# Optimization experiments

Measured on AMD Instinct MI355X. Metric: run time of the kernel, lower is better.

Reference implementation:

```python
import jax, jax.numpy as jnp
import numpy as np

BETA = 0.9
THRESHOLD = 0.9
SIM_TIME = 100

@jax.custom_vjp
def spike(u):
    # snntorch ATan surrogate spike: forward heaviside, backward 1/(1+(pi*u)^2) (alpha=2)
    return (u > 0).astype(u.dtype)

def _spike_fwd(u):
    return (u > 0).astype(u.dtype), u

def _spike_bwd(u, g):
    return (g / (1.0 + (jnp.pi * u) ** 2),)

spike.defvjp(_spike_fwd, _spike_bwd)

def setup_inputs() -> dict:
    key = jax.random.key(0)
    k1, k2, k3 = jax.random.split(key, 3)
    B, D, H = 2048, 1024, 256
    x = jax.random.normal(k1, (B, D), dtype=jnp.float32)
    enc_w = jax.random.normal(k2, (D, H), dtype=jnp.float32) * 0.1
    dec_w = jax.random.normal(k3, (H, D), dtype=jnp.float32) * 0.1
    return {"x": x, "enc_w": enc_w, "dec_w": dec_w}

def _snn_forward(x, enc_w, dec_w):
    B = x.shape[0]
    D, H = enc_w.shape
    dt = x.dtype
    # input current is constant across timesteps (x fixed); hoist the matmul
    in_cur = x @ enc_w  # [B, H]

    def step(carry, _):
        # NOTE: original repo swaps snntorch's (spk, mem) return, so the
        # carried "mem" state is actually the previous spike train, and the
        # membrane potential is what flows into the decoder matmul.
        s_e, s_d, _, _ = carry
        reset_e = jax.lax.stop_gradient((s_e > THRESHOLD).astype(dt))
        m_e = BETA * s_e + in_cur - reset_e * THRESHOLD          # [B, H]
        spk_e = spike(m_e - THRESHOLD)
        out_cur = m_e @ dec_w                                    # [B, D] (mem used as 'spikes')
        reset_d = jax.lax.stop_gradient((s_d > THRESHOLD).astype(dt))
        m_d = BETA * s_d + out_cur - reset_d * THRESHOLD         # [B, D]
        spk_d = spike(m_d - THRESHOLD)
        return (spk_e, spk_d, m_e, m_d), None

    init = (jnp.zeros((B, H), dt), jnp.zeros((B, D), dt),
            jnp.zeros((B, H), dt), jnp.zeros((B, D), dt))
    (s_e, s_d, m_e, m_d), _ = jax.lax.scan(step, init, None, length=SIM_TIME)
    # original returns (spikes_decoder, spikes_encoder) which hold the membranes
    return m_d, m_e

def reference(x, enc_w, dec_w):
    return _snn_forward(x, enc_w, dec_w)
```

## Files before the change

kernel.cpp:

```cpp
#include <hip/hip_runtime.h>


typedef __attribute__((ext_vector_type(8))) short bf16x8;
typedef __attribute__((ext_vector_type(4))) float f32x4;
typedef __attribute__((ext_vector_type(8))) unsigned short ushort8;

__device__ __forceinline__ unsigned short f2bf(float f) {
    unsigned u = __builtin_bit_cast(unsigned, f);
    unsigned r = u + 0x7FFFu + ((u >> 16) & 1u);
    return (unsigned short)(r >> 16);
}

__device__ __forceinline__ void gload_lds16(const void* src, void* dst) {
    __builtin_amdgcn_global_load_lds(
        (const __attribute__((address_space(1))) void*)src,
        (__attribute__((address_space(3))) void*)dst, 16, 0, 0);
}

template <int ROWS>
__device__ __forceinline__ void stage_tile(const unsigned short* __restrict__ g,
                                           int ld, unsigned short* lds, int t) {
    #pragma unroll
    for (int c = 0; c < ROWS / 32; ++c) {
        const int idx = c * 256 + t;
        const int row = idx >> 3;
        const int chunk = (idx & 7) ^ (row & 7);
        const unsigned short* src = g + (size_t)row * ld + chunk * 8;
        unsigned short* dst = lds + (size_t)(idx & ~63) * 8;
        gload_lds16(src, dst);
    }
}

__global__ __launch_bounds__(256) void gemm1_bk256(
    const unsigned short* __restrict__ A,
    const unsigned short* __restrict__ Bt,
    float* __restrict__ C,
    unsigned short* __restrict__ Cbf)
{
    constexpr int N = 256, K = 1024, BK = 256, NT = K / BK;
    __shared__ __align__(16) unsigned short As[2][32 * BK];
    __shared__ __align__(16) unsigned short Bs[2][32 * BK];

    const int t = threadIdx.x;
    const int lane = t & 63;
    const int l15 = lane & 15, l4 = lane >> 4;
    const int wid = t >> 6;
    const int wr = wid >> 1, wc = wid & 1;
    const int brow = blockIdx.y * 32, bcol = blockIdx.x * 32;

    const unsigned short* Ab = A + (size_t)brow * K;
    const unsigned short* Bb = Bt + (size_t)bcol * K;

    auto stage = [&](int kt, int buf) {
        #pragma unroll
        for (int c = 0; c < 4; ++c) {
            const int idx = c * 256 + t;
            const int row = idx >> 5;
            const int ch = (idx & 31) ^ (row & 31);
            gload_lds16(Ab + (size_t)row * K + kt * BK + ch * 8,
                        &As[buf][(idx & ~63) * 8]);
        }
        #pragma unroll
        for (int c = 0; c < 4; ++c) {
            const int idx = c * 256 + t;
            const int row = idx >> 5;
            const int ch = (idx & 31) ^ (row & 31);
            gload_lds16(Bb + (size_t)row * K + kt * BK + ch * 8,
                        &Bs[buf][(idx & ~63) * 8]);
        }
    };

    f32x4 acc = {0.f, 0.f, 0.f, 0.f};
    stage(0, 0);
    for (int kt = 0; kt < NT; ++kt) {
        __syncthreads();
        if (kt + 1 < NT) stage(kt + 1, (kt + 1) & 1);
        const unsigned short* Asb = As[kt & 1];
        const unsigned short* Bsb = Bs[kt & 1];
        const int ra = wr * 16 + l15;
        const int rb = wc * 16 + l15;
        #pragma unroll
        for (int s = 0; s < 8; ++s) {
            const int ca = (s * 4 + l4) ^ (ra & 31);
            const bf16x8 aF = *(const bf16x8*)&Asb[ra * BK + ca * 8];
            const int cb = (s * 4 + l4) ^ (rb & 31);
            const bf16x8 bF = *(const bf16x8*)&Bsb[rb * BK + cb * 8];
            acc = __builtin_amdgcn_mfma_f32_16x16x32_bf16(aF, bF, acc, 0, 0, 0);
        }
    }

    #pragma unroll
    for (int reg = 0; reg < 4; ++reg) {
        const int row = brow + wr * 16 + l4 * 4 + reg;
        const int col = bcol + wc * 16 + l15;
        const float v = acc[reg];
        C[(size_t)row * N + col] = v;
        Cbf[(size_t)row * N + col] = f2bf(v);
    }
}

__global__ __launch_bounds__(256) void gemm2_kres128(
    const unsigned short* __restrict__ A,
    const unsigned short* __restrict__ B,
    float* __restrict__ C)
{
    constexpr int K = 256, N = 1024;
    __shared__ __align__(16) unsigned short As[4][32 * 64];
    __shared__ __align__(16) unsigned short Bs[4][128 * 64];

    const int t = threadIdx.x;
    const int lane = t & 63;
    const int l15 = lane & 15, l4 = lane >> 4;
    const int wid = t >> 6;
    const int wr = wid >> 1, wc = wid & 1;
    const int brow = blockIdx.y * 32, bcol = blockIdx.x * 128;

    #pragma unroll
    for (int kt = 0; kt < 4; ++kt) {
        stage_tile<32>(A + (size_t)brow * K + kt * 64, K, As[kt], t);
        stage_tile<128>(B + (size_t)bcol * K + kt * 64, K, Bs[kt], t);
    }
    __syncthreads();

    f32x4 acc[4];
    #pragma unroll
    for (int j = 0; j < 4; ++j) acc[j] = {0.f, 0.f, 0.f, 0.f};

    #pragma unroll
    for (int kt = 0; kt < 4; ++kt)
        #pragma unroll
        for (int s = 0; s < 2; ++s) {
            const int ra = wr * 16 + l15;
            const int cha = (s * 4 + l4) ^ (ra & 7);
            const bf16x8 aF = *(const bf16x8*)&As[kt][ra * 64 + cha * 8];
            #pragma unroll
            for (int j = 0; j < 4; ++j) {
                const int rb = wc * 64 + j * 16 + l15;
                const int chb = (s * 4 + l4) ^ (rb & 7);
                const bf16x8 bF = *(const bf16x8*)&Bs[kt][rb * 64 + chb * 8];
                acc[j] = __builtin_amdgcn_mfma_f32_16x16x32_bf16(aF, bF, acc[j], 0, 0, 0);
            }
        }

    #pragma unroll
    for (int j = 0; j < 4; ++j)
        #pragma unroll
        for (int reg = 0; reg < 4; ++reg) {
            const int row = brow + wr * 16 + l4 * 4 + reg;
            const int col = bcol + wc * 64 + j * 16 + l15;
            C[(size_t)row * N + col] = acc[j][reg];
        }
}

__global__ __launch_bounds__(256) void prep(
    const float* __restrict__ x, const float* __restrict__ enc,
    const float* __restrict__ dec, unsigned short* __restrict__ x_bf,
    unsigned short* __restrict__ encT, unsigned short* __restrict__ decT)
{
    __shared__ unsigned short tile[32][33];
    const int bid = blockIdx.x;
    const int t = threadIdx.x;

    if (bid < 1024) {
        const int i = bid * 256 + t;
        float4 a = ((const float4*)x)[2 * i];
        float4 b = ((const float4*)x)[2 * i + 1];
        ushort8 v;
        v[0] = f2bf(a.x); v[1] = f2bf(a.y); v[2] = f2bf(a.z); v[3] = f2bf(a.w);
        v[4] = f2bf(b.x); v[5] = f2bf(b.y); v[6] = f2bf(b.z); v[7] = f2bf(b.w);
        ((ushort8*)x_bf)[i] = v;
        return;
    }
    const float* in; unsigned short* out; int R, C, bx, by;
    if (bid < 1280) {
        const int bb = bid - 1024;
        in = enc; out = encT; R = 1024; C = 256; bx = bb % 8; by = bb / 8;
    } else {
        const int bb = bid - 1280;
        in = dec; out = decT; R = 256; C = 1024; bx = bb % 32; by = bb / 32;
    }
    const int r0 = by * 32, c0 = bx * 32;
    const int tx = t % 32, ty = t / 32;
    #pragma unroll
    for (int k = 0; k < 4; ++k) {
        const int lr = ty + k * 8;
        tile[lr][tx] = f2bf(in[(size_t)(r0 + lr) * C + c0 + tx]);
    }
    __syncthreads();
    #pragma unroll
    for (int k = 0; k < 4; ++k) {
        const int lc = ty + k * 8;
        out[(size_t)(c0 + lc) * R + r0 + tx] = tile[tx][lc];
    }
}

#define BKF 32
#define PADF 4
template <int BM, int BN, int TM, int TN>
__global__ __launch_bounds__(256) void gemm_f32(
    const float* __restrict__ A, const float* __restrict__ B,
    float* __restrict__ C, int M, int N, int K)
{
    __shared__ float As[BKF][BM + PADF];
    __shared__ float Bs[BKF][BN + PADF];
    const int t = threadIdx.x;
    const int brow = blockIdx.y * BM, bcol = blockIdx.x * BN;
    constexpr int NTX = BN / TN;
    const int tx = t % NTX, ty = t / NTX;
    float acc[TM][TN];
    #pragma unroll
    for (int i = 0; i < TM; ++i)
        #pragma unroll
        for (int j = 0; j < TN; ++j) acc[i][j] = 0.f;
    for (int k0 = 0; k0 < K; k0 += BKF) {
        #pragma unroll
        for (int v = t; v < BM * BKF / 4; v += 256) {
            const int row = v / (BKF / 4), kv = v % (BKF / 4);
            const float4 val = *(const float4*)&A[(size_t)(brow + row) * K + k0 + kv * 4];
            As[kv * 4 + 0][row] = val.x; As[kv * 4 + 1][row] = val.y;
            As[kv * 4 + 2][row] = val.z; As[kv * 4 + 3][row] = val.w;
        }
        #pragma unroll
        for (int v = t; v < BKF * BN / 4; v += 256) {
            const int kk = v / (BN / 4), cv = v % (BN / 4);
            *(float4*)&Bs[kk][cv * 4] = *(const float4*)&B[(size_t)(k0 + kk) * N + bcol + cv * 4];
        }
        __syncthreads();
        #pragma unroll
        for (int k = 0; k < BKF; ++k) {
            float a[TM], b[TN];
            #pragma unroll
            for (int i = 0; i < TM; ++i) a[i] = As[k][ty * TM + i];
            #pragma unroll
            for (int j = 0; j < TN; ++j) b[j] = Bs[k][tx * TN + j];
            #pragma unroll
            for (int i = 0; i < TM; ++i)
                #pragma unroll
                for (int j = 0; j < TN; ++j) acc[i][j] = fmaf(a[i], b[j], acc[i][j]);
        }
        __syncthreads();
    }
    #pragma unroll
    for (int i = 0; i < TM; ++i)
        #pragma unroll
        for (int j = 0; j < TN; ++j)
            C[(size_t)(brow + ty * TM + i) * N + bcol + tx * TN + j] = acc[i][j];
}

extern "C" void kernel_launch(void* const* d_in, const int* in_sizes, int n_in,
                              void* d_out, int out_size, void* d_ws, size_t ws_size,
                              hipStream_t stream) {
    const float* x     = (const float*)d_in[0];
    const float* enc_w = (const float*)d_in[1];
    const float* dec_w = (const float*)d_in[2];

    const int B = 2048, D = 1024, H = 256;
    float* m_d = (float*)d_out;
    float* m_e = (float*)d_out + (size_t)B * D;

    const size_t need = (size_t)B * D * 2 + (size_t)D * H * 2 * 2 + (size_t)B * H * 2;
    if (ws_size >= need) {
        unsigned short* x_bf  = (unsigned short*)d_ws;
        unsigned short* encT  = x_bf + (size_t)B * D;
        unsigned short* decT  = encT + (size_t)H * D;
        unsigned short* me_bf = decT + (size_t)D * H;

        prep<<<dim3(1536), dim3(256), 0, stream>>>(x, enc_w, dec_w, x_bf, encT, decT);

        gemm1_bk256<<<dim3(H / 32, B / 32), dim3(256), 0, stream>>>(x_bf, encT, m_e, me_bf);
        gemm2_kres128<<<dim3(D / 128, B / 32), dim3(256), 0, stream>>>(me_bf, decT, m_d);
    } else {
        gemm_f32<64, 32, 4, 2><<<dim3(H / 32, B / 64), dim3(256), 0, stream>>>(x, enc_w, m_e, B, H, D);
        gemm_f32<64, 64, 4, 4><<<dim3(D / 64, B / 64), dim3(256), 0, stream>>>(m_e, dec_w, m_d, B, D, H);
    }
}
```

Measured before the change: 23.74 us.

## Fuse both GEMMs into a persistent kernel with per-strip dependency counters

The two GEMM launches become one 512-block kernel. Blocks take work tiles through atomic counters: first the encoder GEMM tiles, then the decoder GEMM tiles. Each decoder tile spins on a per-strip release/acquire counter until that strip's encoder output is complete, which lets the two stages overlap and removes a launch boundary. The cost is an extra memset launch, atomic traffic, a spin-wait dependency, and a larger 80KB static LDS allocation, which may reduce occupancy.

```diff
diff --git a/kernel.cpp b/kernel.cpp
--- a/kernel.cpp
+++ b/kernel.cpp
@@ -31,125 +31,152 @@
     }
 }
 
-__global__ __launch_bounds__(256) void gemm1_bk256(
-    const unsigned short* __restrict__ A,
-    const unsigned short* __restrict__ Bt,
-    float* __restrict__ C,
-    unsigned short* __restrict__ Cbf)
+__global__ __launch_bounds__(256) void fused12(
+    const unsigned short* __restrict__ x_bf,
+    const unsigned short* __restrict__ encT,
+    const unsigned short* __restrict__ decT,
+    float* __restrict__ m_e,
+    unsigned short* __restrict__ me_bf,
+    float* __restrict__ m_d,
+    unsigned int* __restrict__ ctr)
 {
-    constexpr int N = 256, K = 1024, BK = 256, NT = K / BK;
-    __shared__ __align__(16) unsigned short As[2][32 * BK];
-    __shared__ __align__(16) unsigned short Bs[2][32 * BK];
+    __shared__ __align__(16) unsigned char smem[81920];
+    volatile unsigned int* s_t = (volatile unsigned int*)smem;
 
     const int t = threadIdx.x;
     const int lane = t & 63;
     const int l15 = lane & 15, l4 = lane >> 4;
     const int wid = t >> 6;
     const int wr = wid >> 1, wc = wid & 1;
-    const int brow = blockIdx.y * 32, bcol = blockIdx.x * 32;
-
-    const unsigned short* Ab = A + (size_t)brow * K;
-    const unsigned short* Bb = Bt + (size_t)bcol * K;
-
-    auto stage = [&](int kt, int buf) {
-        #pragma unroll
-        for (int c = 0; c < 4; ++c) {
-            const int idx = c * 256 + t;
-            const int row = idx >> 5;
-            const int ch = (idx & 31) ^ (row & 31);
-            gload_lds16(Ab + (size_t)row * K + kt * BK + ch * 8,
-                        &As[buf][(idx & ~63) * 8]);
-        }
-        #pragma unroll
-        for (int c = 0; c < 4; ++c) {
-            const int idx = c * 256 + t;
-            const int row = idx >> 5;
-            const int ch = (idx & 31) ^ (row & 31);
-            gload_lds16(Bb + (size_t)row * K + kt * BK + ch * 8,
-                        &Bs[buf][(idx & ~63) * 8]);
-        }
-    };
-
-    f32x4 acc = {0.f, 0.f, 0.f, 0.f};
-    stage(0, 0);
-    for (int kt = 0; kt < NT; ++kt) {
-        __syncthreads();
-        if (kt + 1 < NT) stage(kt + 1, (kt + 1) & 1);
-        const unsigned short* Asb = As[kt & 1];
-        const unsigned short* Bsb = Bs[kt & 1];
-        const int ra = wr * 16 + l15;
-        const int rb = wc * 16 + l15;
-        #pragma unroll
-        for (int s = 0; s < 8; ++s) {
-            const int ca = (s * 4 + l4) ^ (ra & 31);
-            const bf16x8 aF = *(const bf16x8*)&Asb[ra * BK + ca * 8];
-            const int cb = (s * 4 + l4) ^ (rb & 31);
-            const bf16x8 bF = *(const bf16x8*)&Bsb[rb * BK + cb * 8];
-            acc = __builtin_amdgcn_mfma_f32_16x16x32_bf16(aF, bF, acc, 0, 0, 0);
-        }
-    }
-
-    #pragma unroll
-    for (int reg = 0; reg < 4; ++reg) {
-        const int row = brow + wr * 16 + l4 * 4 + reg;
-        const int col = bcol + wc * 16 + l15;
-        const float v = acc[reg];
-        C[(size_t)row * N + col] = v;
-        Cbf[(size_t)row * N + col] = f2bf(v);
-    }
-}
-
-__global__ __launch_bounds__(256) void gemm2_kres128(
-    const unsigned short* __restrict__ A,
-    const unsigned short* __restrict__ B,
-    float* __restrict__ C)
-{
-    constexpr int K = 256, N = 1024;
-    __shared__ __align__(16) unsigned short As[4][32 * 64];
-    __shared__ __align__(16) unsigned short Bs[4][128 * 64];
-
-    const int t = threadIdx.x;
-    const int lane = t & 63;
-    const int l15 = lane & 15, l4 = lane >> 4;
-    const int wid = t >> 6;
-    const int wr = wid >> 1, wc = wid & 1;
-    const int brow = blockIdx.y * 32, bcol = blockIdx.x * 128;
-
-    #pragma unroll
-    for (int kt = 0; kt < 4; ++kt) {
-        stage_tile<32>(A + (size_t)brow * K + kt * 64, K, As[kt], t);
-        stage_tile<128>(B + (size_t)bcol * K + kt * 64, K, Bs[kt], t);
-    }
-    __syncthreads();
-
-    f32x4 acc[4];
-    #pragma unroll
-    for (int j = 0; j < 4; ++j) acc[j] = {0.f, 0.f, 0.f, 0.f};
-
-    #pragma unroll
-    for (int kt = 0; kt < 4; ++kt)
-        #pragma unroll
-        for (int s = 0; s < 2; ++s) {
-            const int ra = wr * 16 + l15;
-            const int cha = (s * 4 + l4) ^ (ra & 7);
-            const bf16x8 aF = *(const bf16x8*)&As[kt][ra * 64 + cha * 8];
-            #pragma unroll
-            for (int j = 0; j < 4; ++j) {
-                const int rb = wc * 64 + j * 16 + l15;
-                const int chb = (s * 4 + l4) ^ (rb & 7);
-                const bf16x8 bF = *(const bf16x8*)&Bs[kt][rb * 64 + chb * 8];
-                acc[j] = __builtin_amdgcn_mfma_f32_16x16x32_bf16(aF, bF, acc[j], 0, 0, 0);
+
+    {
+        unsigned short* As1 = (unsigned short*)smem;
+        unsigned short* Bs1 = (unsigned short*)(smem + 32768);
+        constexpr int K = 1024, N = 256, BK = 256, NT = K / BK;
+        for (;;) {
+            __syncthreads();
+            if (t == 0) *s_t = atomicAdd(&ctr[0], 1u);
+            __syncthreads();
+            const unsigned int T = *s_t;
+            __syncthreads();
+            if (T >= 512u) break;
+            const int strip = (int)(T >> 3);
+            const int brow = strip * 32, bcol = (int)(T & 7u) * 32;
+            const unsigned short* Ab = x_bf + (size_t)brow * K;
+            const unsigned short* Bb = encT + (size_t)bcol * K;
+
+            auto stage = [&](int kt, int buf) {
+                #pragma unroll
+                for (int c = 0; c < 4; ++c) {
+                    const int idx = c * 256 + t;
+                    const int row = idx >> 5;
+                    const int ch = (idx & 31) ^ (row & 31);
+                    gload_lds16(Ab + (size_t)row * K + kt * BK + ch * 8,
+                                As1 + buf * 8192 + (idx & ~63) * 8);
+                }
+                #pragma unroll
+                for (int c = 0; c < 4; ++c) {
+                    const int idx = c * 256 + t;
+                    const int row = idx >> 5;
+                    const int ch = (idx & 31) ^ (row & 31);
+                    gload_lds16(Bb + (size_t)row * K + kt * BK + ch * 8,
+                                Bs1 + buf * 8192 + (idx & ~63) * 8);
+                }
+            };
+
+            f32x4 acc = {0.f, 0.f, 0.f, 0.f};
+            stage(0, 0);
+            for (int kt = 0; kt < NT; ++kt) {
+                __syncthreads();
+                if (kt + 1 < NT) stage(kt + 1, (kt + 1) & 1);
+                const unsigned short* Asb = As1 + (kt & 1) * 8192;
+                const unsigned short* Bsb = Bs1 + (kt & 1) * 8192;
+                const int ra = wr * 16 + l15;
+                const int rb = wc * 16 + l15;
+                #pragma unroll
+                for (int s = 0; s < 8; ++s) {
+                    const int ca = (s * 4 + l4) ^ (ra & 31);
+                    const bf16x8 aF = *(const bf16x8*)&Asb[ra * BK + ca * 8];
+                    const int cb = (s * 4 + l4) ^ (rb & 31);
+                    const bf16x8 bF = *(const bf16x8*)&Bsb[rb * BK + cb * 8];
+                    acc = __builtin_amdgcn_mfma_f32_16x16x32_bf16(aF, bF, acc, 0, 0, 0);
+                }
             }
-        }
-
-    #pragma unroll
-    for (int j = 0; j < 4; ++j)
-        #pragma unroll
-        for (int reg = 0; reg < 4; ++reg) {
-            const int row = brow + wr * 16 + l4 * 4 + reg;
-            const int col = bcol + wc * 64 + j * 16 + l15;
-            C[(size_t)row * N + col] = acc[j][reg];
-        }
+            #pragma unroll
+            for (int reg = 0; reg < 4; ++reg) {
+                const int row = brow + wr * 16 + l4 * 4 + reg;
+                const int col = bcol + wc * 16 + l15;
+                const float v = acc[reg];
+                m_e[(size_t)row * N + col] = v;
+                me_bf[(size_t)row * N + col] = f2bf(v);
+            }
+            __syncthreads();
+            if (t == 0)
+                __hip_atomic_fetch_add(&ctr[2 + strip], 1u,
+                                       __ATOMIC_RELEASE, __HIP_MEMORY_SCOPE_AGENT);
+        }
+    }
+
+    {
+        unsigned short* As2 = (unsigned short*)smem;
+        unsigned short* Bs2 = (unsigned short*)(smem + 16384);
+        constexpr int K = 256, N = 1024;
+        for (;;) {
+            __syncthreads();
+            if (t == 0) *s_t = atomicAdd(&ctr[1], 1u);
+            __syncthreads();
+            const unsigned int U = *s_t;
+            __syncthreads();
+            if (U >= 512u) break;
+            const int strip = (int)(U >> 3);
+            const int brow = strip * 32, bcol = (int)(U & 7u) * 128;
+
+            #pragma unroll
+            for (int kt = 0; kt < 4; ++kt)
+                stage_tile<128>(decT + (size_t)bcol * K + kt * 64, K,
+                                Bs2 + kt * 8192, t);
+
+            if (t == 0) {
+                while (__hip_atomic_load(&ctr[2 + strip], __ATOMIC_ACQUIRE,
+                                         __HIP_MEMORY_SCOPE_AGENT) < 8u)
+                    __builtin_amdgcn_s_sleep(2);
+            }
+            __syncthreads();
+
+            #pragma unroll
+            for (int kt = 0; kt < 4; ++kt)
+                stage_tile<32>(me_bf + (size_t)brow * K + kt * 64, K,
+                               As2 + kt * 2048, t);
+            __syncthreads();
+
+            f32x4 acc[4];
+            #pragma unroll
+            for (int j = 0; j < 4; ++j) acc[j] = {0.f, 0.f, 0.f, 0.f};
+            #pragma unroll
+            for (int kt = 0; kt < 4; ++kt)
+                #pragma unroll
+                for (int s = 0; s < 2; ++s) {
+                    const int ra = wr * 16 + l15;
+                    const int cha = (s * 4 + l4) ^ (ra & 7);
+                    const bf16x8 aF = *(const bf16x8*)&As2[kt * 2048 + ra * 64 + cha * 8];
+                    #pragma unroll
+                    for (int j = 0; j < 4; ++j) {
+                        const int rb = wc * 64 + j * 16 + l15;
+                        const int chb = (s * 4 + l4) ^ (rb & 7);
+                        const bf16x8 bF = *(const bf16x8*)&Bs2[kt * 8192 + rb * 64 + chb * 8];
+                        acc[j] = __builtin_amdgcn_mfma_f32_16x16x32_bf16(aF, bF, acc[j], 0, 0, 0);
+                    }
+                }
+            #pragma unroll
+            for (int j = 0; j < 4; ++j)
+                #pragma unroll
+                for (int reg = 0; reg < 4; ++reg) {
+                    const int row = brow + wr * 16 + l4 * 4 + reg;
+                    const int col = bcol + wc * 64 + j * 16 + l15;
+                    m_d[(size_t)row * N + col] = acc[j][reg];
+                }
+        }
+    }
 }
 
 __global__ __launch_bounds__(256) void prep(
@@ -258,17 +285,21 @@
     float* m_d = (float*)d_out;
     float* m_e = (float*)d_out + (size_t)B * D;
 
-    const size_t need = (size_t)B * D * 2 + (size_t)D * H * 2 * 2 + (size_t)B * H * 2;
+    const size_t buf_bytes = (size_t)B * D * 2 + (size_t)D * H * 2 * 2
+                           + (size_t)B * H * 2;
+    const size_t ctr_off = (buf_bytes + 255) & ~(size_t)255;
+    const size_t need = ctr_off + 66 * sizeof(unsigned int);
     if (ws_size >= need) {
         unsigned short* x_bf  = (unsigned short*)d_ws;
         unsigned short* encT  = x_bf + (size_t)B * D;
         unsigned short* decT  = encT + (size_t)H * D;
         unsigned short* me_bf = decT + (size_t)D * H;
-
+        unsigned int*   ctr   = (unsigned int*)((char*)d_ws + ctr_off);
+
+        hipMemsetAsync(ctr, 0, 66 * sizeof(unsigned int), stream);
         prep<<<dim3(1536), dim3(256), 0, stream>>>(x, enc_w, dec_w, x_bf, encT, decT);
-
-        gemm1_bk256<<<dim3(H / 32, B / 32), dim3(256), 0, stream>>>(x_bf, encT, m_e, me_bf);
-        gemm2_kres128<<<dim3(D / 128, B / 32), dim3(256), 0, stream>>>(me_bf, decT, m_d);
+        fused12<<<dim3(512), dim3(256), 0, stream>>>(x_bf, encT, decT,
+                                                     m_e, me_bf, m_d, ctr);
     } else {
         gemm_f32<64, 32, 4, 2><<<dim3(H / 32, B / 64), dim3(256), 0, stream>>>(x, enc_w, m_e, B, H, D);
         gemm_f32<64, 64, 4, 4><<<dim3(D / 64, B / 64), dim3(256), 0, stream>>>(m_e, dec_w, m_d, B, D, H);
```

New measurement: 69.37 us. +192.2%, slower.
